# Kernel tuning notes

Measured on AMD Instinct MI355X. Metric: run time of the kernel, lower is better.

Reference implementation:

```python
import jax, jax.numpy as jnp
import numpy as np

LN_EPS = 1e-6


def setup_inputs() -> dict:
    key = jax.random.key(0)
    ks = jax.random.split(key, 8)
    B, L, D = 8, 4096, 1024
    s = 1.0 / np.sqrt(D)
    inputs = jax.random.normal(ks[0], (B, L, D), dtype=jnp.float32)
    # PositionwiseFeedForward params (d_ff == d_model here)
    w1 = jax.random.normal(ks[1], (D, D), dtype=jnp.float32) * s
    b1 = jnp.zeros((D,), dtype=jnp.float32)
    w2 = jax.random.normal(ks[2], (D, D), dtype=jnp.float32) * s
    b2 = jnp.zeros((D,), dtype=jnp.float32)
    ln_g = jnp.ones((D,), dtype=jnp.float32)
    ln_b = jnp.zeros((D,), dtype=jnp.float32)
    # gating layer: Linear(2D, 2D)
    wg = jax.random.normal(ks[3], (2 * D, 2 * D), dtype=jnp.float32) * (1.0 / np.sqrt(2 * D))
    bg = jnp.zeros((2 * D,), dtype=jnp.float32)
    return {"inputs": inputs, "w1": w1, "b1": b1, "w2": w2, "b2": b2,
            "ln_g": ln_g, "ln_b": ln_b, "wg": wg, "bg": bg}


def _layer_norm(x, g, b):
    mu = jnp.mean(x, axis=-1, keepdims=True)
    var = jnp.mean(jnp.square(x - mu), axis=-1, keepdims=True)
    return (x - mu) * jax.lax.rsqrt(var + LN_EPS) * g + b


def reference(inputs, w1, b1, w2, b2, ln_g, ln_b, wg, bg):
    B, L, D = inputs.shape
    # Cumulative average: identical math to tril(ones)/arange mask @ inputs,
    # computed in O(L) via prefix sum instead of an O(L^2) matmul.
    denom = jnp.arange(1, L + 1, dtype=inputs.dtype)[:, None]  # [L,1]
    avg = jnp.cumsum(inputs, axis=1) / denom                    # [B,L,D]
    # PositionwiseFeedForward (eval mode, dropout=0): LN -> relu(Linear) -> Linear -> +residual
    h = _layer_norm(avg, ln_g, ln_b)
    inter = jax.nn.relu(jnp.einsum('bld,df->blf', h, w1) + b1)
    avg_out = jnp.einsum('blf,fd->bld', inter, w2) + b2 + avg
    # Gating: Linear on concat(inputs, avg_out), split, sigmoid gates
    concat = jnp.concatenate([inputs, avg_out], axis=-1)        # [B,L,2D]
    gates = jnp.einsum('ble,ef->blf', concat, wg) + bg          # [B,L,2D]
    input_gate, forget_gate = gates[..., :D], gates[..., D:]
    out = jax.nn.sigmoid(input_gate) * inputs + jax.nn.sigmoid(forget_gate) * avg_out
    return out
```

## Files before the change

kernel.cpp:

```cpp
#include <hip/hip_runtime.h>

typedef __bf16 bf16_t;
typedef bf16_t bf16x8 __attribute__((ext_vector_type(8)));
typedef bf16_t bf16x4 __attribute__((ext_vector_type(4)));
typedef float  f32x4  __attribute__((ext_vector_type(4)));

typedef const __attribute__((address_space(1))) void* gptr_t;
typedef __attribute__((address_space(3))) void* sptr_t;

#define BATCH 8
#define SEQL  4096
#define DIM   1024
#define MROWS 32768

__device__ __forceinline__ float sigmoidf_(float v) {
    return 1.0f / (1.0f + __expf(-v));
}

template <int PERM>
__global__ void transpose_cast(const float* __restrict__ W, bf16_t* __restrict__ WT,
                               int K, int N) {
    __shared__ float s[32][33];
    int tx = threadIdx.x, ty = threadIdx.y;
    int x = blockIdx.x * 32 + tx;
    int y = blockIdx.y * 32 + ty;
    s[ty][tx] = W[(size_t)y * N + x];
    __syncthreads();
    int n = blockIdx.x * 32 + ty;
    int k = blockIdx.y * 32 + tx;
    int nd = n;
    if (PERM) {
        if (n < 1024) nd = ((n >> 6) << 7) + (n & 63);
        else          nd = (((n - 1024) >> 6) << 7) + 64 + ((n - 1024) & 63);
    }
    WT[(size_t)nd * K + k] = (bf16_t)s[tx][ty];
}

__global__ void scan_chunks(const float* __restrict__ x, float* __restrict__ cs) {
    int tid = threadIdx.x;
    int b = blockIdx.x >> 6, c = blockIdx.x & 63;
    const f32x4* x4 = (const f32x4*)x;
    size_t base = ((size_t)b * SEQL + (size_t)c * 64) * 256 + tid;
    f32x4 s0 = {0.f, 0.f, 0.f, 0.f}, s1 = {0.f, 0.f, 0.f, 0.f};
#pragma unroll 8
    for (int j = 0; j < 64; j += 2) {
        s0 += x4[base + (size_t)j * 256];
        s1 += x4[base + (size_t)(j + 1) * 256];
    }
    ((f32x4*)cs)[((size_t)(b << 6) + c) * 256 + tid] = s0 + s1;
}

__global__ void scan_prefix(float* __restrict__ cs) {
    int t = blockIdx.x * 256 + threadIdx.x;
    int b = t >> 10, d = t & 1023;
    size_t base = (size_t)(b << 6) * 1024 + d;
    float v[64];
#pragma unroll
    for (int c = 0; c < 64; ++c) v[c] = cs[base + (size_t)c * 1024];
    float run = 0.f;
#pragma unroll
    for (int c = 0; c < 64; ++c) {
        float tv = v[c];
        cs[base + (size_t)c * 1024] = run;
        run += tv;
    }
}

__global__ __launch_bounds__(256) void scan_ln(
    const float* __restrict__ x, const float* __restrict__ cs,
    const float* __restrict__ g, const float* __restrict__ bb,
    float* __restrict__ avg, bf16_t* __restrict__ hb, bf16_t* __restrict__ xb) {
    int tid = threadIdx.x;
    int wave = tid >> 6, lane = tid & 63;
    int b = blockIdx.x >> 6, c = blockIdx.x & 63;
    __shared__ float red[8];
    const f32x4* x4 = (const f32x4*)x;
    f32x4* avg4 = (f32x4*)avg;
    bf16x4* hb4 = (bf16x4*)hb;
    bf16x4* xb4 = (bf16x4*)xb;
    f32x4 run = ((const f32x4*)cs)[((size_t)(b << 6) + c) * 256 + tid];
    f32x4 gv = ((const f32x4*)g)[tid];
    f32x4 bv = ((const f32x4*)bb)[tid];
    size_t row0 = (size_t)b * SEQL + (size_t)c * 64;
    f32x4 xv = x4[row0 * 256 + tid];
    for (int j = 0; j < 64; ++j) {
        size_t ridx = (row0 + j) * 256 + tid;
        f32x4 xnext = {0.f, 0.f, 0.f, 0.f};
        if (j < 63) xnext = x4[ridx + 256];
        run += xv;
        float inv = 1.0f / (float)(c * 64 + j + 1);
        f32x4 av = run * inv;
        avg4[ridx] = av;
        bf16x4 xo = { (bf16_t)xv[0], (bf16_t)xv[1], (bf16_t)xv[2], (bf16_t)xv[3] };
        xb4[ridx] = xo;
        float s  = av[0] + av[1] + av[2] + av[3];
        float sq = av[0]*av[0] + av[1]*av[1] + av[2]*av[2] + av[3]*av[3];
#pragma unroll
        for (int off = 32; off; off >>= 1) {
            s  += __shfl_xor(s, off);
            sq += __shfl_xor(sq, off);
        }
        if (lane == 0) { red[wave] = s; red[4 + wave] = sq; }
        __syncthreads();
        s  = red[0] + red[1] + red[2] + red[3];
        sq = red[4] + red[5] + red[6] + red[7];
        float mu  = s * (1.f / DIM);
        float var = sq * (1.f / DIM) - mu * mu;
        var = var < 0.f ? 0.f : var;
        float rs = 1.0f / sqrtf(var + 1e-6f);
        f32x4 hn = (av - mu) * rs * gv + bv;
        bf16x4 ho = { (bf16_t)hn[0], (bf16_t)hn[1], (bf16_t)hn[2], (bf16_t)hn[3] };
        hb4[ridx] = ho;
        __syncthreads();
        xv = xnext;
    }
}

template <int EPI>
__global__ __launch_bounds__(256, 2) void gemm_bt(
    const bf16_t* __restrict__ A0, const bf16_t* __restrict__ A1, int kSplit,
    const bf16_t* __restrict__ Bt, int N, int K,
    const float* __restrict__ bias, const float* __restrict__ addsrc,
    const float* __restrict__ xsrc,
    float* __restrict__ outf, bf16_t* __restrict__ outb) {
    __shared__ char smem[73728];
    const int tid = threadIdx.x;
    const int wave = tid >> 6, lane = tid & 63;

    const int nwg = gridDim.x;
    const int q8 = nwg >> 3;
    const int lid = (blockIdx.x & 7) * q8 + ((int)blockIdx.x >> 3);
    const int nBlocks = N >> 7;
    const int m0 = (lid / nBlocks) << 8;
    const int n0 = (lid % nBlocks) << 7;
    const int wm = (wave >> 1) << 7;
    const int wn = (wave & 1) << 6;
    const int lrow16 = lane & 15;
    const int ksw = (((lane >> 4) ^ ((lane >> 1) & 3)) << 3);

    f32x4 acc[8][4] = {};

    auto stageA = [&](int kt, int buf) {
        int k0 = kt << 5;
        if (k0 > K - 32) k0 = K - 32;
        const bf16_t* Asrc; int ak0;
        if (k0 < kSplit) { Asrc = A0; ak0 = k0; }
        else             { Asrc = A1; ak0 = k0 - kSplit; }
        char* base = smem + buf * 24576;
#pragma unroll
        for (int rd = 0; rd < 4; ++rd) {
            int ci = tid + (rd << 8);
            int row = ci >> 2, ch = ci & 3;
            int chs = ch ^ ((row >> 1) & 3);
            const bf16_t* gp = Asrc + (size_t)(m0 + row) * kSplit + ak0 + (chs << 3);
            bf16_t* sb = (bf16_t*)base + (size_t)(ci & ~63) * 8;
            __builtin_amdgcn_global_load_lds((gptr_t)gp, (sptr_t)sb, 16, 0, 0);
        }
    };
    auto stageB = [&](int kt, int buf) {
        int k0 = kt << 5;
        if (k0 > K - 32) k0 = K - 32;
        char* base = smem + buf * 24576 + 16384;
#pragma unroll
        for (int rd = 0; rd < 2; ++rd) {
            int ci = tid + (rd << 8);
            int row = ci >> 2, ch = ci & 3;
            int chs = ch ^ ((row >> 1) & 3);
            const bf16_t* gp = Bt + (size_t)(n0 + row) * K + k0 + (chs << 3);
            bf16_t* sb = (bf16_t*)base + (size_t)(ci & ~63) * 8;
            __builtin_amdgcn_global_load_lds((gptr_t)gp, (sptr_t)sb, 16, 0, 0);
        }
    };

    bf16x8 af[4], bfv[4];
    auto readA4 = [&](int buf, int half) {
        const bf16_t* As_ = (const bf16_t*)(smem + buf * 24576);
#pragma unroll
        for (int mi = 0; mi < 4; ++mi)
            af[mi] = *(const bf16x8*)&As_[(wm + (half * 4 + mi) * 16 + lrow16) * 32 + ksw];
    };
    auto readB4 = [&](int buf) {
        const bf16_t* Bs_ = (const bf16_t*)(smem + buf * 24576 + 16384);
#pragma unroll
        for (int ni = 0; ni < 4; ++ni)
            bfv[ni] = *(const bf16x8*)&Bs_[(wn + ni * 16 + lrow16) * 32 + ksw];
    };
    auto mfma16 = [&](int half) {
        __builtin_amdgcn_s_setprio(1);
#pragma unroll
        for (int mi = 0; mi < 4; ++mi)
#pragma unroll
            for (int ni = 0; ni < 4; ++ni)
                acc[half * 4 + mi][ni] = __builtin_amdgcn_mfma_f32_16x16x32_bf16(
                    af[mi], bfv[ni], acc[half * 4 + mi][ni], 0, 0, 0);
        __builtin_amdgcn_s_setprio(0);
    };

#define BAR_  __builtin_amdgcn_s_barrier()
#define SB_   __builtin_amdgcn_sched_barrier(0)
#define LG0_  asm volatile("s_waitcnt lgkmcnt(0)" ::: "memory")
#define VMW6_ asm volatile("s_waitcnt vmcnt(6)" ::: "memory")

    stageA(0, 0); stageB(0, 0);
    stageA(1, 1); stageB(1, 1);
    VMW6_;
    BAR_;

    const int nT = K >> 5;
    int cb = 0, st = 2;
#pragma nounroll
    for (int t = 0; t < nT; ++t) {
        readB4(cb); readA4(cb, 0);
        stageA(t + 2, st);
        BAR_; LG0_; SB_; mfma16(0); BAR_;
        readA4(cb, 1);
        stageB(t + 2, st);
        VMW6_;
        BAR_; LG0_; SB_; mfma16(1); BAR_;
        cb = (cb == 2) ? 0 : cb + 1;
        st = (st == 2) ? 0 : st + 1;
    }
    asm volatile("s_waitcnt vmcnt(0)" ::: "memory");

#undef BAR_
#undef SB_
#undef LG0_
#undef VMW6_

    const int erow = (lane >> 4) << 2;

    if (EPI == 4) {
        __syncthreads();
        float* xch = (float*)smem;
        const int T = n0 >> 7;
        if (wn) {
#pragma unroll
            for (int mi = 0; mi < 8; ++mi) {
#pragma unroll
                for (int ni = 0; ni < 4; ++ni) {
                    int dc = ni * 16 + lrow16;
                    float bcol = bias[1024 + T * 64 + dc];
                    int d = T * 64 + dc;
#pragma unroll
                    for (int r = 0; r < 4; ++r) {
                        int rowW = mi * 16 + erow + r;
                        int row = m0 + wm + rowW;
                        float v = acc[mi][ni][r] + bcol;
                        int sw = ((rowW >> 2) & 1) << 4;
                        xch[(wm + rowW) * 64 + (dc ^ sw)] =
                            sigmoidf_(v) * addsrc[(size_t)row * 1024 + d];
                    }
                }
            }
        }
        __syncthreads();
        if (!wn) {
#pragma unroll
            for (int mi = 0; mi < 8; ++mi) {
#pragma unroll
                for (int ni = 0; ni < 4; ++ni) {
                    int dc = ni * 16 + lrow16;
                    float bcol = bias[T * 64 + dc];
                    int d = T * 64 + dc;
#pragma unroll
                    for (int r = 0; r < 4; ++r) {
                        int rowW = mi * 16 + erow + r;
                        int row = m0 + wm + rowW;
                        float v = acc[mi][ni][r] + bcol;
                        int sw = ((rowW >> 2) & 1) << 4;
                        float tot = sigmoidf_(v) * xsrc[(size_t)row * 1024 + d]
                                  + xch[(wm + rowW) * 64 + (dc ^ sw)];
                        outf[(size_t)row * 1024 + d] = tot;
                    }
                }
            }
        }
        return;
    }

#pragma unroll
    for (int mi = 0; mi < 8; ++mi) {
#pragma unroll
        for (int ni = 0; ni < 4; ++ni) {
            int col = n0 + wn + ni * 16 + lrow16;
            float bcol = bias[col];
#pragma unroll
            for (int r = 0; r < 4; ++r) {
                int row = m0 + wm + mi * 16 + erow + r;
                size_t idx = (size_t)row * N + col;
                float v = acc[mi][ni][r];
                if (EPI == 1) {
                    v += bcol;
                    v = v > 0.f ? v : 0.f;
                    outb[idx] = (bf16_t)v;
                } else {
                    v += bcol + addsrc[idx];
                    outf[idx] = v;
                    outb[idx] = (bf16_t)v;
                }
            }
        }
    }
}

extern "C" void kernel_launch(void* const* d_in, const int* in_sizes, int n_in,
                              void* d_out, int out_size, void* d_ws, size_t ws_size,
                              hipStream_t stream) {
    const float* inp  = (const float*)d_in[0];
    const float* w1   = (const float*)d_in[1];
    const float* b1   = (const float*)d_in[2];
    const float* w2   = (const float*)d_in[3];
    const float* b2   = (const float*)d_in[4];
    const float* ln_g = (const float*)d_in[5];
    const float* ln_b = (const float*)d_in[6];
    const float* wg   = (const float*)d_in[7];
    const float* bg   = (const float*)d_in[8];
    float* out = (float*)d_out;

    char* w = (char*)d_ws;
    float*  avg    = (float*)w;   w += (size_t)MROWS * DIM * 4;
    float*  avgout = (float*)w;   w += (size_t)MROWS * DIM * 4;
    bf16_t* xb     = (bf16_t*)w;  w += (size_t)MROWS * DIM * 2;
    bf16_t* hb     = (bf16_t*)w;  w += (size_t)MROWS * DIM * 2;
    bf16_t* interb = (bf16_t*)w;  w += (size_t)MROWS * DIM * 2;
    bf16_t* w1t    = (bf16_t*)w;  w += (size_t)DIM * DIM * 2;
    bf16_t* w2t    = (bf16_t*)w;  w += (size_t)DIM * DIM * 2;
    bf16_t* wgt    = (bf16_t*)w;  w += (size_t)2 * DIM * 2 * DIM * 2;
    float*  csum   = (float*)w;   w += (size_t)BATCH * 64 * DIM * 4;
    bf16_t* aob    = hb;

    transpose_cast<0><<<dim3(32, 32), dim3(32, 32), 0, stream>>>(w1, w1t, DIM, DIM);
    transpose_cast<0><<<dim3(32, 32), dim3(32, 32), 0, stream>>>(w2, w2t, DIM, DIM);
    transpose_cast<1><<<dim3(64, 64), dim3(32, 32), 0, stream>>>(wg, wgt, 2 * DIM, 2 * DIM);

    scan_chunks<<<BATCH * 64, 256, 0, stream>>>(inp, csum);
    scan_prefix<<<32, 256, 0, stream>>>(csum);
    scan_ln<<<BATCH * 64, 256, 0, stream>>>(inp, csum, ln_g, ln_b, avg, hb, xb);

    gemm_bt<1><<<(MROWS / 256) * (DIM / 128), 256, 0, stream>>>(
        hb, hb, DIM, w1t, DIM, DIM, b1, nullptr, nullptr, nullptr, interb);

    gemm_bt<2><<<(MROWS / 256) * (DIM / 128), 256, 0, stream>>>(
        interb, interb, DIM, w2t, DIM, DIM, b2, avg, nullptr, avgout, aob);

    gemm_bt<4><<<(MROWS / 256) * (2 * DIM / 128), 256, 0, stream>>>(
        xb, aob, DIM, wgt, 2 * DIM, 2 * DIM, bg, avgout, inp, out, nullptr);
}
```

Baseline: 927.2 us.

## Shrink GEMM tiles to 128x128 with double-buffered LDS pipeline

Shrinks the GEMM workgroup tile from 256x128 to 128x128, which halves accumulator registers and LDS (73.7 KB to 32 KB). It raises the launch bound to 3 workgroups per CU. The three-stage K-loop, with its two half-steps, becomes a two-stage double buffer with a single MFMA phase per step. The aim is higher occupancy and latency hiding, at the cost of lower data reuse per tile, double the number of workgroups, and less prefetch depth.

```diff
diff --git a/kernel.cpp b/kernel.cpp
--- a/kernel.cpp
+++ b/kernel.cpp
@@ -117,13 +117,13 @@
 }
 
 template <int EPI>
-__global__ __launch_bounds__(256, 2) void gemm_bt(
+__global__ __launch_bounds__(256, 3) void gemm_bt(
     const bf16_t* __restrict__ A0, const bf16_t* __restrict__ A1, int kSplit,
     const bf16_t* __restrict__ Bt, int N, int K,
     const float* __restrict__ bias, const float* __restrict__ addsrc,
     const float* __restrict__ xsrc,
     float* __restrict__ outf, bf16_t* __restrict__ outb) {
-    __shared__ char smem[73728];
+    __shared__ char smem[32768];
     const int tid = threadIdx.x;
     const int wave = tid >> 6, lane = tid & 63;
 
@@ -131,14 +131,14 @@
     const int q8 = nwg >> 3;
     const int lid = (blockIdx.x & 7) * q8 + ((int)blockIdx.x >> 3);
     const int nBlocks = N >> 7;
-    const int m0 = (lid / nBlocks) << 8;
+    const int m0 = (lid / nBlocks) << 7;
     const int n0 = (lid % nBlocks) << 7;
-    const int wm = (wave >> 1) << 7;
+    const int wm = (wave >> 1) << 6;
     const int wn = (wave & 1) << 6;
     const int lrow16 = lane & 15;
     const int ksw = (((lane >> 4) ^ ((lane >> 1) & 3)) << 3);
 
-    f32x4 acc[8][4] = {};
+    f32x4 acc[4][4] = {};
 
     auto stageA = [&](int kt, int buf) {
         int k0 = kt << 5;
@@ -146,9 +146,9 @@
         const bf16_t* Asrc; int ak0;
         if (k0 < kSplit) { Asrc = A0; ak0 = k0; }
         else             { Asrc = A1; ak0 = k0 - kSplit; }
-        char* base = smem + buf * 24576;
-#pragma unroll
-        for (int rd = 0; rd < 4; ++rd) {
+        char* base = smem + (buf << 14);
+#pragma unroll
+        for (int rd = 0; rd < 2; ++rd) {
             int ci = tid + (rd << 8);
             int row = ci >> 2, ch = ci & 3;
             int chs = ch ^ ((row >> 1) & 3);
@@ -160,7 +160,7 @@
     auto stageB = [&](int kt, int buf) {
         int k0 = kt << 5;
         if (k0 > K - 32) k0 = K - 32;
-        char* base = smem + buf * 24576 + 16384;
+        char* base = smem + (buf << 14) + 8192;
 #pragma unroll
         for (int rd = 0; rd < 2; ++rd) {
             int ci = tid + (rd << 8);
@@ -173,59 +173,58 @@
     };
 
     bf16x8 af[4], bfv[4];
-    auto readA4 = [&](int buf, int half) {
-        const bf16_t* As_ = (const bf16_t*)(smem + buf * 24576);
-#pragma unroll
-        for (int mi = 0; mi < 4; ++mi)
-            af[mi] = *(const bf16x8*)&As_[(wm + (half * 4 + mi) * 16 + lrow16) * 32 + ksw];
-    };
-    auto readB4 = [&](int buf) {
-        const bf16_t* Bs_ = (const bf16_t*)(smem + buf * 24576 + 16384);
+    auto readAB = [&](int buf) {
+        const bf16_t* As_ = (const bf16_t*)(smem + (buf << 14));
+        const bf16_t* Bs_ = As_ + 4096;
 #pragma unroll
         for (int ni = 0; ni < 4; ++ni)
             bfv[ni] = *(const bf16x8*)&Bs_[(wn + ni * 16 + lrow16) * 32 + ksw];
+#pragma unroll
+        for (int mi = 0; mi < 4; ++mi)
+            af[mi] = *(const bf16x8*)&As_[(wm + mi * 16 + lrow16) * 32 + ksw];
     };
-    auto mfma16 = [&](int half) {
+    auto mfma16 = [&]() {
         __builtin_amdgcn_s_setprio(1);
 #pragma unroll
         for (int mi = 0; mi < 4; ++mi)
 #pragma unroll
             for (int ni = 0; ni < 4; ++ni)
-                acc[half * 4 + mi][ni] = __builtin_amdgcn_mfma_f32_16x16x32_bf16(
-                    af[mi], bfv[ni], acc[half * 4 + mi][ni], 0, 0, 0);
+                acc[mi][ni] = __builtin_amdgcn_mfma_f32_16x16x32_bf16(
+                    af[mi], bfv[ni], acc[mi][ni], 0, 0, 0);
         __builtin_amdgcn_s_setprio(0);
     };
 
 #define BAR_  __builtin_amdgcn_s_barrier()
 #define SB_   __builtin_amdgcn_sched_barrier(0)
 #define LG0_  asm volatile("s_waitcnt lgkmcnt(0)" ::: "memory")
-#define VMW6_ asm volatile("s_waitcnt vmcnt(6)" ::: "memory")
+#define VMW4_ asm volatile("s_waitcnt vmcnt(4)" ::: "memory")
 
     stageA(0, 0); stageB(0, 0);
     stageA(1, 1); stageB(1, 1);
-    VMW6_;
+    VMW4_;
     BAR_;
 
     const int nT = K >> 5;
-    int cb = 0, st = 2;
+    int cb = 0;
 #pragma nounroll
     for (int t = 0; t < nT; ++t) {
-        readB4(cb); readA4(cb, 0);
-        stageA(t + 2, st);
-        BAR_; LG0_; SB_; mfma16(0); BAR_;
-        readA4(cb, 1);
-        stageB(t + 2, st);
-        VMW6_;
-        BAR_; LG0_; SB_; mfma16(1); BAR_;
-        cb = (cb == 2) ? 0 : cb + 1;
-        st = (st == 2) ? 0 : st + 1;
+        readAB(cb);
+        LG0_;
+        BAR_;
+        stageA(t + 2, cb);
+        stageB(t + 2, cb);
+        SB_;
+        mfma16();
+        VMW4_;
+        BAR_;
+        cb ^= 1;
     }
     asm volatile("s_waitcnt vmcnt(0)" ::: "memory");
 
 #undef BAR_
 #undef SB_
 #undef LG0_
-#undef VMW6_
+#undef VMW4_
 
     const int erow = (lane >> 4) << 2;
 
@@ -235,7 +234,7 @@
         const int T = n0 >> 7;
         if (wn) {
 #pragma unroll
-            for (int mi = 0; mi < 8; ++mi) {
+            for (int mi = 0; mi < 4; ++mi) {
 #pragma unroll
                 for (int ni = 0; ni < 4; ++ni) {
                     int dc = ni * 16 + lrow16;
@@ -256,7 +255,7 @@
         __syncthreads();
         if (!wn) {
 #pragma unroll
-            for (int mi = 0; mi < 8; ++mi) {
+            for (int mi = 0; mi < 4; ++mi) {
 #pragma unroll
                 for (int ni = 0; ni < 4; ++ni) {
                     int dc = ni * 16 + lrow16;
@@ -279,7 +278,7 @@
     }
 
 #pragma unroll
-    for (int mi = 0; mi < 8; ++mi) {
+    for (int mi = 0; mi < 4; ++mi) {
 #pragma unroll
         for (int ni = 0; ni < 4; ++ni) {
             int col = n0 + wn + ni * 16 + lrow16;
@@ -337,12 +336,12 @@
     scan_prefix<<<32, 256, 0, stream>>>(csum);
     scan_ln<<<BATCH * 64, 256, 0, stream>>>(inp, csum, ln_g, ln_b, avg, hb, xb);
 
-    gemm_bt<1><<<(MROWS / 256) * (DIM / 128), 256, 0, stream>>>(
+    gemm_bt<1><<<(MROWS / 128) * (DIM / 128), 256, 0, stream>>>(
         hb, hb, DIM, w1t, DIM, DIM, b1, nullptr, nullptr, nullptr, interb);
 
-    gemm_bt<2><<<(MROWS / 256) * (DIM / 128), 256, 0, stream>>>(
+    gemm_bt<2><<<(MROWS / 128) * (DIM / 128), 256, 0, stream>>>(
         interb, interb, DIM, w2t, DIM, DIM, b2, avg, nullptr, avgout, aob);
 
-    gemm_bt<4><<<(MROWS / 256) * (2 * DIM / 128), 256, 0, stream>>>(
+    gemm_bt<4><<<(MROWS / 128) * (2 * DIM / 128), 256, 0, stream>>>(
         xb, aob, DIM, wgt, 2 * DIM, 2 * DIM, bg, avgout, inp, out, nullptr);
 }
```

Result: slower. 985.4 us (+6.3%).
